# Performance work log

Hardware: AMD Instinct MI355X
Metric: run time of the kernel (lower is better)

The kernel has to match this reference:

```python
import jax, jax.numpy as jnp
import numpy as np

NGRAM_SIZE = 3
MFCC_COV_FEAT_LENGTH = 91
MFCC_COV_NUM = 6
NUM_CHANNEL = 4
CHOSEN_FEAT = [547, 548, 549, 551, 554, 556, 557, 558, 559, 560, 561, 562, 563, 565,
               566, 567, 570, 576, 580, 581, 582, 583, 584, 585, 588, 593, 598, 599, 600]
POS = {f: i for i, f in enumerate(CHOSEN_FEAT)}

D = 10000   # out_dimension
L = 100     # levels
T = 2048    # time steps


def setup_inputs() -> dict:
    key = jax.random.key(0)
    ks = jax.random.split(key, 8)
    signals = jax.random.uniform(ks[0], (T, NUM_CHANNEL), dtype=jnp.float32)
    feat = jax.random.normal(ks[1], (600,), dtype=jnp.float32)
    # Random / Level embeddings are bipolar {-1,+1} hypervectors
    keys_hv = jnp.where(jax.random.uniform(ks[2], (NUM_CHANNEL, D)) < 0.5, -1.0, 1.0).astype(jnp.float32)
    level_weight = jnp.where(jax.random.uniform(ks[3], (L, D)) < 0.5, -1.0, 1.0).astype(jnp.float32)
    # 29 Sinusoid(1, D) kernels stacked: weight [29, D], bias [29, D] ~ U(0, 2pi)
    feat_w = jax.random.normal(ks[4], (len(CHOSEN_FEAT), D), dtype=jnp.float32)
    feat_b = jax.random.uniform(ks[5], (len(CHOSEN_FEAT), D), dtype=jnp.float32, maxval=2.0 * np.pi)
    # 6 Sinusoid(91, D) kernels stacked: weight [6, D, 91], bias [6, D]
    mfcc_w = jax.random.normal(ks[6], (MFCC_COV_NUM, D, MFCC_COV_FEAT_LENGTH), dtype=jnp.float32)
    mfcc_b = jax.random.uniform(ks[7], (MFCC_COV_NUM, D), dtype=jnp.float32, maxval=2.0 * np.pi)
    return dict(signals=signals, feat=feat, keys_hv=keys_hv, level_weight=level_weight,
                feat_w=feat_w, feat_b=feat_b, mfcc_w=mfcc_w, mfcc_b=mfcc_b)


def _forward(signals, feat, keys_hv, level_weight, feat_w, feat_b, mfcc_w, mfcc_b):
    Lv = level_weight.shape[0]
    # Level embedding: nearest level of value clamped to [0,1]
    idx = jnp.clip(jnp.round(jnp.clip(signals, 0.0, 1.0) * (Lv - 1)).astype(jnp.int32), 0, Lv - 1)
    embedded = level_weight[idx]                        # [T, C, D]
    # generic encoding: bind channel keys, multiset over channels
    per_t = jnp.sum(keys_hv[None, :, :] * embedded, axis=1)  # [T, D]
    # n-gram binding with permute (= roll along D)
    n = NGRAM_SIZE
    Tn = per_t.shape[0] - n + 1
    ngram = jnp.roll(per_t[0:Tn], n - 1, axis=-1)
    for i in range(1, n - 1):
        ngram = ngram * jnp.roll(per_t[i:Tn + i], n - 1 - i, axis=-1)
    ngram = ngram * per_t[n - 1:Tn + n - 1]             # [T-n+1, D]
    sample_hv = jnp.sum(ngram, axis=0)                  # multiset -> [D]

    # 29 scalar Sinusoid kernels: feat_hvs[f] uses feat[f-1]
    sel = feat[jnp.array([f - 1 for f in CHOSEN_FEAT])]          # [29]
    proj = sel[:, None] * feat_w                                  # [29, D]
    fhv = jnp.cos(proj + feat_b) * jnp.sin(proj)                  # [29, D]
    h = lambda f: fhv[POS[f]]

    # 6 MFCC Sinusoid kernels, multibind (product) over the 6 HVs
    mf = feat[:MFCC_COV_NUM * MFCC_COV_FEAT_LENGTH].reshape(MFCC_COV_NUM, MFCC_COV_FEAT_LENGTH)
    mproj = jnp.einsum('kdf,kf->kd', mfcc_w, mf)                  # [6, D]
    mhv = jnp.cos(mproj + mfcc_b) * jnp.sin(mproj)
    mfcc_hv = jnp.prod(mhv, axis=0)                               # [D]

    comb = (h(547) * h(559) * h(565)
            + h(548) * h(560) * h(566)
            + h(549) * h(561) * h(567)
            + h(551) * h(554)
            + h(556) * h(558) * h(584) * h(557) * h(585) * h(581) * h(580)
              * h(582) * h(583) * h(598) * h(600) * h(599)
            + h(562) + h(563)
            + h(570) * h(588)
            + h(576) + h(593)
            + mfcc_hv)
    sample_hv = sample_hv * comb
    # hard_quantize
    return jnp.where(sample_hv > 0, 1.0, -1.0).astype(sample_hv.dtype).ravel()


def reference(signals, feat, keys_hv, level_weight, feat_w, feat_b, mfcc_w, mfcc_b):
    return _forward(signals, feat, keys_hv, level_weight, feat_w, feat_b, mfcc_w, mfcc_b)
```

## Files before the change

### kernel.cpp

```cpp
#include <hip/hip_runtime.h>
#include <stdint.h>

#define D 10000
#define LVL 100
#define T 2048
#define TN 2046
#define NW 162
#define NCHUNK 32

#define WS_ACC 0
#define WS_MHV (D)
#define WS_IDX_BYTES (7 * D * 4)

__global__ __launch_bounds__(256) void k1_prep(
    const float* __restrict__ signals,
    const float* __restrict__ feat,
    const float* __restrict__ mfcc_w,
    const float* __restrict__ mfcc_b,
    float* __restrict__ ws)
{
    int gid = blockIdx.x * 256 + threadIdx.x;
    float* acc = ws + WS_ACC;
    float* mhv = ws + WS_MHV;
    unsigned char* idxb = (unsigned char*)ws + WS_IDX_BYTES;

    if (gid < D) acc[gid] = 0.f;

    if (gid < T * 4) {
        float s = signals[gid];
        s = fminf(fmaxf(s, 0.f), 1.f);
        float v = rintf(s * 99.0f);
        int iv = (int)v;
        iv = iv < 0 ? 0 : (iv > 99 ? 99 : iv);
        idxb[gid] = (unsigned char)iv;
    }

    if (gid < 6 * D) {
        int k = gid / D;
        const float* wp = mfcc_w + (size_t)gid * 91;
        const float* mf = feat + k * 91;
        float s = 0.f;
        #pragma unroll 7
        for (int f = 0; f < 91; ++f) s = fmaf(wp[f], mf[f], s);
        float b = mfcc_b[gid];
        mhv[gid] = cosf(s + b) * sinf(s);
    }
}

__global__ __launch_bounds__(64) void k2_ngram(
    const float* __restrict__ keys,
    const float* __restrict__ lw,
    float* __restrict__ ws)
{
    float* acc = ws + WS_ACC;
    const uint32_t* idxw = (const uint32_t*)((const unsigned char*)ws + WS_IDX_BYTES);

    int w = blockIdx.x;
    int chunk = blockIdx.y;
    int l = threadIdx.x;
    int t0 = chunk * 64;
    int len = min(64, TN - t0);

    int rc = (w * 62 + l + (D - 2)) % D;
    float k0 = keys[rc];
    float k1 = keys[D + rc];
    float k2 = keys[2 * D + rc];
    float k3 = keys[3 * D + rc];

    auto row = [&](int t) -> float {
        uint32_t iw = idxw[t];
        int l0 = iw & 0xff;
        int l1 = (iw >> 8) & 0xff;
        int l2 = (iw >> 16) & 0xff;
        int l3 = (iw >> 24);
        float r = k0 * lw[l0 * D + rc];
        r = fmaf(k1, lw[l1 * D + rc], r);
        r = fmaf(k2, lw[l2 * D + rc], r);
        r = fmaf(k3, lw[l3 * D + rc], r);
        return r;
    };

    float a = row(t0);
    float b = row(t0 + 1);
    float accv = 0.f;
    for (int t = t0; t < t0 + len; ++t) {
        float c = row(t + 2);
        float a2 = __shfl_up(a, 2, 64);
        float b1 = __shfl_up(b, 1, 64);
        accv = fmaf(a2 * b1, c, accv);
        a = b; b = c;
    }
    int outcol = w * 62 + l - 2;
    if (l >= 2 && outcol < D) atomicAdd(&acc[outcol], accv);
}

__global__ __launch_bounds__(256) void k3_finish(
    const float* __restrict__ feat,
    const float* __restrict__ feat_w,
    const float* __restrict__ feat_b,
    float* __restrict__ out,
    const float* __restrict__ ws)
{
    static const int CF[29] = {547,548,549,551,554,556,557,558,559,560,561,562,563,565,
                               566,567,570,576,580,581,582,583,584,585,588,593,598,599,600};
    int d = blockIdx.x * 256 + threadIdx.x;
    if (d >= D) return;
    const float* acc = ws + WS_ACC;
    const float* mhv = ws + WS_MHV;

    float h[29];
    #pragma unroll
    for (int i = 0; i < 29; ++i) {
        float sel = feat[CF[i] - 1];
        float proj = sel * feat_w[i * D + d];
        h[i] = cosf(proj + feat_b[i * D + d]) * sinf(proj);
    }

    float mf = mhv[d];
    #pragma unroll
    for (int k = 1; k < 6; ++k) mf *= mhv[k * D + d];

    float comb = h[0] * h[8] * h[13]
               + h[1] * h[9] * h[14]
               + h[2] * h[10] * h[15]
               + h[3] * h[4]
               + h[5] * h[7] * h[22] * h[6] * h[23] * h[19] * h[18]
                 * h[20] * h[21] * h[26] * h[28] * h[27]
               + h[11] + h[12]
               + h[16] * h[24]
               + h[17] + h[25]
               + mf;

    float sv = acc[d] * comb;
    out[d] = sv > 0.f ? 1.f : -1.f;
}

extern "C" void kernel_launch(void* const* d_in, const int* in_sizes, int n_in,
                              void* d_out, int out_size, void* d_ws, size_t ws_size,
                              hipStream_t stream) {
    const float* signals = (const float*)d_in[0];
    const float* feat    = (const float*)d_in[1];
    const float* keys    = (const float*)d_in[2];
    const float* lw      = (const float*)d_in[3];
    const float* feat_w  = (const float*)d_in[4];
    const float* feat_b  = (const float*)d_in[5];
    const float* mfcc_w  = (const float*)d_in[6];
    const float* mfcc_b  = (const float*)d_in[7];
    float* ws  = (float*)d_ws;
    float* out = (float*)d_out;

    k1_prep<<<dim3(235), dim3(256), 0, stream>>>(signals, feat, mfcc_w, mfcc_b, ws);
    k2_ngram<<<dim3(NW, NCHUNK), dim3(64), 0, stream>>>(keys, lw, ws);
    k3_finish<<<dim3(40), dim3(256), 0, stream>>>(feat, feat_w, feat_b, out, ws);
}
```

Baseline: 131.0 us.

## Fuse prep and n-gram kernels, replace atomics with per-chunk partial sums

Merges the index-quantization and MFCC projection work into the n-gram kernel: each n-gram block quantizes its own signal rows into shared memory, and extra blocks compute the MFCC hypervectors. Atomic accumulation is replaced by per-chunk partial sums written to workspace and reduced in the finish kernel, which also drops the zero-init. Chunk length doubles to 128 with unrolling, the MFCC dot product uses float4 loads, and the finish kernel now launches 64-thread blocks. This removes one launch and the atomics in exchange for redundant quantization work per block and a 16-way reduction in the final kernel.

```diff
diff --git a/kernel.cpp b/kernel.cpp
--- a/kernel.cpp
+++ b/kernel.cpp
@@ -2,99 +2,121 @@
 #include <stdint.h>
 
 #define D 10000
-#define LVL 100
 #define T 2048
 #define TN 2046
 #define NW 162
-#define NCHUNK 32
+#define NCHUNK 16
+#define TCHUNK 128
+#define NGBLK (NW * NCHUNK)
+#define MHVTH (6 * D)
+#define MHVBLK ((MHVTH + 63) / 64)
 
-#define WS_ACC 0
-#define WS_MHV (D)
-#define WS_IDX_BYTES (7 * D * 4)
 
-__global__ __launch_bounds__(256) void k1_prep(
+__global__ __launch_bounds__(64) void kA(
     const float* __restrict__ signals,
     const float* __restrict__ feat,
+    const float* __restrict__ keys,
+    const float* __restrict__ lw,
     const float* __restrict__ mfcc_w,
     const float* __restrict__ mfcc_b,
     float* __restrict__ ws)
 {
-    int gid = blockIdx.x * 256 + threadIdx.x;
-    float* acc = ws + WS_ACC;
-    float* mhv = ws + WS_MHV;
-    unsigned char* idxb = (unsigned char*)ws + WS_IDX_BYTES;
+    const int bid = blockIdx.x;
+    const int l   = threadIdx.x;
 
-    if (gid < D) acc[gid] = 0.f;
+    if (bid < NGBLK) {
+        __shared__ uint32_t sidx[TCHUNK + 2];
+        const int w     = bid % NW;
+        const int chunk = bid / NW;
+        const int t0    = chunk * TCHUNK;
+        const int len   = min(TCHUNK, TN - t0);
+        const int rows  = len + 2;
 
-    if (gid < T * 4) {
-        float s = signals[gid];
-        s = fminf(fmaxf(s, 0.f), 1.f);
-        float v = rintf(s * 99.0f);
-        int iv = (int)v;
-        iv = iv < 0 ? 0 : (iv > 99 ? 99 : iv);
-        idxb[gid] = (unsigned char)iv;
-    }
+        for (int i = l; i < rows; i += 64) {
+            const float4 s = ((const float4*)signals)[t0 + i];
+            uint32_t iw;
+            {
+                float x0 = rintf(fminf(fmaxf(s.x, 0.f), 1.f) * 99.0f);
+                float x1 = rintf(fminf(fmaxf(s.y, 0.f), 1.f) * 99.0f);
+                float x2 = rintf(fminf(fmaxf(s.z, 0.f), 1.f) * 99.0f);
+                float x3 = rintf(fminf(fmaxf(s.w, 0.f), 1.f) * 99.0f);
+                iw  = (uint32_t)(int)x0;
+                iw |= (uint32_t)(int)x1 << 8;
+                iw |= (uint32_t)(int)x2 << 16;
+                iw |= (uint32_t)(int)x3 << 24;
+            }
+            sidx[i] = iw;
+        }
+        __syncthreads();
 
-    if (gid < 6 * D) {
-        int k = gid / D;
-        const float* wp = mfcc_w + (size_t)gid * 91;
-        const float* mf = feat + k * 91;
-        float s = 0.f;
-        #pragma unroll 7
-        for (int f = 0; f < 91; ++f) s = fmaf(wp[f], mf[f], s);
-        float b = mfcc_b[gid];
-        mhv[gid] = cosf(s + b) * sinf(s);
+        const int rc = (w * 62 + l + (D - 2)) % D;
+        const float k0 = keys[rc];
+        const float k1 = keys[D + rc];
+        const float k2 = keys[2 * D + rc];
+        const float k3 = keys[3 * D + rc];
+
+        auto row = [&](int i) -> float {
+            const uint32_t iw = sidx[i];
+            const int l0 = iw & 0xff;
+            const int l1 = (iw >> 8) & 0xff;
+            const int l2 = (iw >> 16) & 0xff;
+            const int l3 = iw >> 24;
+            float r = k0 * lw[l0 * D + rc];
+            r = fmaf(k1, lw[l1 * D + rc], r);
+            r = fmaf(k2, lw[l2 * D + rc], r);
+            r = fmaf(k3, lw[l3 * D + rc], r);
+            return r;
+        };
+
+        float a = row(0);
+        float b = row(1);
+        float accv = 0.f;
+        if (len == TCHUNK) {
+            #pragma unroll 4
+            for (int i = 0; i < TCHUNK; ++i) {
+                const float c = row(i + 2);
+                const float a2 = __shfl_up(a, 2, 64);
+                const float b1 = __shfl_up(b, 1, 64);
+                accv = fmaf(a2 * b1, c, accv);
+                a = b; b = c;
+            }
+        } else {
+            for (int i = 0; i < len; ++i) {
+                const float c = row(i + 2);
+                const float a2 = __shfl_up(a, 2, 64);
+                const float b1 = __shfl_up(b, 1, 64);
+                accv = fmaf(a2 * b1, c, accv);
+                a = b; b = c;
+            }
+        }
+        const int outcol = w * 62 + l - 2;
+        if (l >= 2 && outcol < D) ws[chunk * D + outcol] = accv;
+    } else {
+        const int gid = (bid - NGBLK) * 64 + l;
+        if (gid < MHVTH) {
+            const int k = gid / D;
+            const float* __restrict__ mf   = feat + k * 91;
+            const float* __restrict__ wrow = mfcc_w + (size_t)gid * 91;
+            const int p = (4 - ((gid * 91) & 3)) & 3;
+            float s = 0.f;
+            for (int f = 0; f < p; ++f) s = fmaf(wrow[f], mf[f], s);
+            const float4* __restrict__ v = (const float4*)(wrow + p);
+            #pragma unroll 2
+            for (int j = 0; j < 22; ++j) {
+                const float4 x = v[j];
+                const int f0 = p + 4 * j;
+                s = fmaf(x.x, mf[f0],     s);
+                s = fmaf(x.y, mf[f0 + 1], s);
+                s = fmaf(x.z, mf[f0 + 2], s);
+                s = fmaf(x.w, mf[f0 + 3], s);
+            }
+            for (int f = p + 88; f < 91; ++f) s = fmaf(wrow[f], mf[f], s);
+            ws[NCHUNK * D + gid] = cosf(s + mfcc_b[gid]) * sinf(s);
+        }
     }
 }
 
-__global__ __launch_bounds__(64) void k2_ngram(
-    const float* __restrict__ keys,
-    const float* __restrict__ lw,
-    float* __restrict__ ws)
-{
-    float* acc = ws + WS_ACC;
-    const uint32_t* idxw = (const uint32_t*)((const unsigned char*)ws + WS_IDX_BYTES);
-
-    int w = blockIdx.x;
-    int chunk = blockIdx.y;
-    int l = threadIdx.x;
-    int t0 = chunk * 64;
-    int len = min(64, TN - t0);
-
-    int rc = (w * 62 + l + (D - 2)) % D;
-    float k0 = keys[rc];
-    float k1 = keys[D + rc];
-    float k2 = keys[2 * D + rc];
-    float k3 = keys[3 * D + rc];
-
-    auto row = [&](int t) -> float {
-        uint32_t iw = idxw[t];
-        int l0 = iw & 0xff;
-        int l1 = (iw >> 8) & 0xff;
-        int l2 = (iw >> 16) & 0xff;
-        int l3 = (iw >> 24);
-        float r = k0 * lw[l0 * D + rc];
-        r = fmaf(k1, lw[l1 * D + rc], r);
-        r = fmaf(k2, lw[l2 * D + rc], r);
-        r = fmaf(k3, lw[l3 * D + rc], r);
-        return r;
-    };
-
-    float a = row(t0);
-    float b = row(t0 + 1);
-    float accv = 0.f;
-    for (int t = t0; t < t0 + len; ++t) {
-        float c = row(t + 2);
-        float a2 = __shfl_up(a, 2, 64);
-        float b1 = __shfl_up(b, 1, 64);
-        accv = fmaf(a2 * b1, c, accv);
-        a = b; b = c;
-    }
-    int outcol = w * 62 + l - 2;
-    if (l >= 2 && outcol < D) atomicAdd(&acc[outcol], accv);
-}
-
-__global__ __launch_bounds__(256) void k3_finish(
+__global__ __launch_bounds__(64) void kB(
     const float* __restrict__ feat,
     const float* __restrict__ feat_w,
     const float* __restrict__ feat_b,
@@ -103,35 +125,38 @@
 {
     static const int CF[29] = {547,548,549,551,554,556,557,558,559,560,561,562,563,565,
                                566,567,570,576,580,581,582,583,584,585,588,593,598,599,600};
-    int d = blockIdx.x * 256 + threadIdx.x;
+    const int d = blockIdx.x * 64 + threadIdx.x;
     if (d >= D) return;
-    const float* acc = ws + WS_ACC;
-    const float* mhv = ws + WS_MHV;
+
+    float acc = 0.f;
+    #pragma unroll
+    for (int c = 0; c < NCHUNK; ++c) acc += ws[c * D + d];
+
+    const float* __restrict__ mhv = ws + NCHUNK * D;
+    float mfp = mhv[d];
+    #pragma unroll
+    for (int k = 1; k < 6; ++k) mfp *= mhv[k * D + d];
 
     float h[29];
     #pragma unroll
     for (int i = 0; i < 29; ++i) {
-        float sel = feat[CF[i] - 1];
-        float proj = sel * feat_w[i * D + d];
+        const float sel  = feat[CF[i] - 1];
+        const float proj = sel * feat_w[i * D + d];
         h[i] = cosf(proj + feat_b[i * D + d]) * sinf(proj);
     }
 
-    float mf = mhv[d];
-    #pragma unroll
-    for (int k = 1; k < 6; ++k) mf *= mhv[k * D + d];
+    const float comb = h[0] * h[8] * h[13]
+                     + h[1] * h[9] * h[14]
+                     + h[2] * h[10] * h[15]
+                     + h[3] * h[4]
+                     + h[5] * h[7] * h[22] * h[6] * h[23] * h[19] * h[18]
+                       * h[20] * h[21] * h[26] * h[28] * h[27]
+                     + h[11] + h[12]
+                     + h[16] * h[24]
+                     + h[17] + h[25]
+                     + mfp;
 
-    float comb = h[0] * h[8] * h[13]
-               + h[1] * h[9] * h[14]
-               + h[2] * h[10] * h[15]
-               + h[3] * h[4]
-               + h[5] * h[7] * h[22] * h[6] * h[23] * h[19] * h[18]
-                 * h[20] * h[21] * h[26] * h[28] * h[27]
-               + h[11] + h[12]
-               + h[16] * h[24]
-               + h[17] + h[25]
-               + mf;
-
-    float sv = acc[d] * comb;
+    const float sv = acc * comb;
     out[d] = sv > 0.f ? 1.f : -1.f;
 }
 
@@ -149,7 +174,7 @@
     float* ws  = (float*)d_ws;
     float* out = (float*)d_out;
 
-    k1_prep<<<dim3(235), dim3(256), 0, stream>>>(signals, feat, mfcc_w, mfcc_b, ws);
-    k2_ngram<<<dim3(NW, NCHUNK), dim3(64), 0, stream>>>(keys, lw, ws);
-    k3_finish<<<dim3(40), dim3(256), 0, stream>>>(feat, feat_w, feat_b, out, ws);
+    kA<<<dim3(NGBLK + MHVBLK), dim3(64), 0, stream>>>(signals, feat, keys, lw,
+                                                      mfcc_w, mfcc_b, ws);
+    kB<<<dim3((D + 63) / 64), dim3(64), 0, stream>>>(feat, feat_w, feat_b, out, ws);
 }
```

Measured after the change: 130.1 us. About the same (-0.7%).
